# Optimization experiments

Hardware: AMD Instinct MI355X
Metric: run time of the kernel (lower is better)

The kernel has to match this reference:

```python
import jax, jax.numpy as jnp
import numpy as np

N, E, C, H, W = 5000, 80000, 32, 8, 8


def setup_inputs() -> dict:
    key = jax.random.key(0)
    k1, k2, k3, k4, k5, k6 = jax.random.split(key, 6)
    h = jax.random.normal(k1, (N, C, H, W), dtype=jnp.float32)
    e = jax.random.uniform(k2, (E,), dtype=jnp.float32)
    src = jax.random.randint(k3, (E,), 0, N, dtype=jnp.int32)
    # ensure every node receives at least one message (avoids -inf segments),
    # matching a connected graph where update_all covers all nodes
    dst = jnp.concatenate([jnp.arange(N, dtype=jnp.int32),
                           jax.random.randint(k4, (E - N,), 0, N, dtype=jnp.int32)])
    fan_in = C * 3 * 3
    bound = float(1.0 / np.sqrt(fan_in))
    conv_w = jax.random.uniform(k5, (C, C, 3, 3), minval=-bound, maxval=bound, dtype=jnp.float32)
    conv_b = jax.random.uniform(k6, (C,), minval=-bound, maxval=bound, dtype=jnp.float32)
    return {"h": h, "e": e, "conv_w": conv_w, "conv_b": conv_b, "src": src, "dst": dst}


def reference(h, e, conv_w, conv_b, src, dst):
    # message: gather source features per edge, scale by scalar edge weight
    m = e[:, None, None, None] * h[src]                      # [E, C, H, W]
    # conv2d(dim->dim, k=3, pad=1) + exact GELU, edges as batch dim
    m = jax.lax.conv_general_dilated(
        m, conv_w, window_strides=(1, 1), padding='SAME',
        dimension_numbers=('NCHW', 'OIHW', 'NCHW'))
    m = jax.nn.gelu(m + conv_b[None, :, None, None], approximate=False)
    # reduce: ragged max over each destination node's mailbox
    out = jax.ops.segment_max(m, dst, num_segments=h.shape[0])  # [N, C, H, W]
    return out
```

## Files before the change

kernel.cpp:

```cpp
#include <hip/hip_runtime.h>
#include <math.h>

#define CCH   32
#define HWPIX 64
#define CHW   2048
#define NHALF 2500
#define HT_STRIDE 40
#define HT_NODE   2600

typedef __attribute__((ext_vector_type(8))) short bf16x8;
typedef __attribute__((ext_vector_type(4))) float f32x4;
typedef unsigned int uint_t;
typedef unsigned short ushort_t;

__device__ __forceinline__ ushort_t f2bf(float f) {
    uint_t u = __float_as_uint(f);
    u += 0x7fffu + ((u >> 16) & 1u);
    return (ushort_t)(u >> 16);
}

__device__ __forceinline__ float fgelu(float x) {
    float x2 = x * x;
    float t = x * fmaf(0.0713548162726f, x2, 1.5957691216f);
    float ez = __expf(-t);
    return x * __builtin_amdgcn_rcpf(1.0f + ez);
}


__global__ __launch_bounds__(256) void hist_prep_kernel(
    const int* __restrict__ dst, int* cnt, int ne, int nhist,
    const float* __restrict__ w, ushort_t* __restrict__ wfrag) {
    int b = blockIdx.x;
    if (b < nhist) {
        int i = b * 256 + threadIdx.x;
        if (i < ne) atomicAdd(&cnt[dst[i]], 1);
    } else {
        for (int idx = threadIdx.x; idx < 18 * 64; idx += 256) {
            int ch = idx / (9 * 64);
            int rem = idx % (9 * 64);
            int tap = rem / 64;
            int l = rem % 64;
            int co = ch * 16 + (l & 15);
            int g = l >> 4;
            for (int j = 0; j < 8; j++) {
                int ci = g * 8 + j;
                wfrag[(size_t)idx * 8 + j] = f2bf(w[(co * CCH + ci) * 9 + tap]);
            }
        }
    }
}

__global__ __launch_bounds__(256) void scan_kernel(const int* __restrict__ cnt,
                                                   int* __restrict__ offs,
                                                   int* __restrict__ cursor,
                                                   int nn) {
    __shared__ int part[256];
    int t = threadIdx.x;
    int per = (nn + 255) >> 8;
    if (per > 32) per = 32;
    int base = t * per;
    int local[32];
    int sum = 0;
    for (int i = 0; i < per; i++) {
        int idx = base + i;
        int v = (idx < nn) ? cnt[idx] : 0;
        local[i] = sum;
        sum += v;
    }
    part[t] = sum;
    __syncthreads();
    int acc = sum;
    for (int d = 1; d < 256; d <<= 1) {
        int tv = (t >= d) ? part[t - d] : 0;
        __syncthreads();
        acc += tv;
        part[t] = acc;
        __syncthreads();
    }
    int excl = acc - sum;
    for (int i = 0; i < per; i++) {
        int idx = base + i;
        if (idx < nn) {
            int o = excl + local[i];
            offs[idx] = o;
            cursor[idx] = o;
        }
    }
    if (t == 255) offs[nn] = acc;
}

__global__ __launch_bounds__(256) void conv_scatter_kernel(
    const float* __restrict__ h, const ushort_t* __restrict__ wfrag,
    ushort_t* __restrict__ convh, int nconv,
    const int* __restrict__ dst, const int* __restrict__ src,
    const float* __restrict__ e, int* cursor, int2* __restrict__ swA, int ne) {
    __shared__ ushort_t Ht[2 * HT_NODE];
    int b = blockIdx.x;
    int t = threadIdx.x;

    if (b >= nconv) {
        int i = (b - nconv) * 256 + t;
        if (i < ne) {
            int p = atomicAdd(&cursor[dst[i]], 1);
            int2 v;
            v.x = src[i];
            v.y = __float_as_int(e[i]);
            swA[p] = v;
        }
        return;
    }

    int node0 = b * 2;
    uint_t* Hd = (uint_t*)Ht;
#pragma unroll
    for (int nd = 0; nd < 2; nd++) {
        const float* hn = h + (size_t)(node0 + nd) * CHW;
#pragma unroll
        for (int it = 0; it < 4; it++) {
            int ci2 = it * 4 + (t >> 6);
            int p = t & 63;
            float a = hn[ci2 * 128 + p];
            float bb = hn[ci2 * 128 + 64 + p];
            uint_t val = (uint_t)f2bf(a) | ((uint_t)f2bf(bb) << 16);
            Hd[nd * (HT_NODE / 2) + p * (HT_STRIDE / 2) + ci2] = val;
        }
    }
    if (t < 40) Hd[0 * (HT_NODE / 2) + 64 * (HT_STRIDE / 2) + (t % 20)] = 0;
    if (t >= 40 && t < 80) Hd[1 * (HT_NODE / 2) + 64 * (HT_STRIDE / 2) + (t - 40) % 20] = 0;
    __syncthreads();

    int l = t & 63;
    int w = __builtin_amdgcn_readfirstlane(t >> 6);
    int nd = w >> 1;
    int ch = w & 1;
    int s = l & 15, g = l >> 4;
    int n = node0 + nd;

    bf16x8 A[9];
#pragma unroll
    for (int tap = 0; tap < 9; tap++)
        A[tap] = ((const bf16x8*)wfrag)[(ch * 9 + tap) * 64 + l];

    f32x4 C[4];
#pragma unroll
    for (int i = 0; i < 4; i++) C[i] = (f32x4){0.f, 0.f, 0.f, 0.f};

    const short* HtS = (const short*)(Ht + nd * HT_NODE);
#pragma unroll
    for (int tau = 0; tau < 4; tau++) {
        int p = tau * 16 + s;
        int y = p >> 3, x = p & 7;
#pragma unroll
        for (int tap = 0; tap < 9; tap++) {
            int dy = tap / 3 - 1, dx = tap % 3 - 1;
            int yy = y + dy, xx = x + dx;
            bool valid = (yy >= 0) & (yy < 8) & (xx >= 0) & (xx < 8);
            int pp = valid ? (yy * 8 + xx) : 64;
            bf16x8 B = *(const bf16x8*)&HtS[pp * HT_STRIDE + g * 8];
            C[tau] = __builtin_amdgcn_mfma_f32_16x16x32_bf16(A[tap], B, C[tau], 0, 0, 0);
        }
    }

    ushort_t* outn = convh + (size_t)n * CHW;
#pragma unroll
    for (int tau = 0; tau < 4; tau++) {
        uint_t lo = (uint_t)f2bf(C[tau][0]) | ((uint_t)f2bf(C[tau][1]) << 16);
        uint_t hi = (uint_t)f2bf(C[tau][2]) | ((uint_t)f2bf(C[tau][3]) << 16);
        uint2 v; v.x = lo; v.y = hi;
        *(uint2*)(outn + (tau * 16 + s) * 32 + ch * 16 + g * 4) = v;
    }
}

__device__ __forceinline__ void red8(float* mn, float* mx, uint4 q, float wg) {
    uint_t u0 = q.x, u1 = q.y, u2 = q.z, u3 = q.w;
    float v;
    v = wg * __uint_as_float(u0 << 16);          mn[0] = fminf(mn[0], v); mx[0] = fmaxf(mx[0], v);
    v = wg * __uint_as_float(u0 & 0xffff0000u);  mn[1] = fminf(mn[1], v); mx[1] = fmaxf(mx[1], v);
    v = wg * __uint_as_float(u1 << 16);          mn[2] = fminf(mn[2], v); mx[2] = fmaxf(mx[2], v);
    v = wg * __uint_as_float(u1 & 0xffff0000u);  mn[3] = fminf(mn[3], v); mx[3] = fmaxf(mx[3], v);
    v = wg * __uint_as_float(u2 << 16);          mn[4] = fminf(mn[4], v); mx[4] = fmaxf(mx[4], v);
    v = wg * __uint_as_float(u2 & 0xffff0000u);  mn[5] = fminf(mn[5], v); mx[5] = fmaxf(mx[5], v);
    v = wg * __uint_as_float(u3 << 16);          mn[6] = fminf(mn[6], v); mx[6] = fmaxf(mx[6], v);
    v = wg * __uint_as_float(u3 & 0xffff0000u);  mn[7] = fminf(mn[7], v); mx[7] = fmaxf(mx[7], v);
}

__global__ __launch_bounds__(256) void gather_max_kernel(
    const ushort_t* __restrict__ convh, const float* __restrict__ bias,
    const int* __restrict__ offs, const int2* __restrict__ swA,
    float* __restrict__ out) {
    int t = threadIdx.x;
    int l = t & 63;
    int w = t >> 6;
    int b = blockIdx.x;
    int q = b & 3;
    int half = (b >> 2) & 1;
    int n = half * NHALF + (b >> 3) * 4 + w;
    int beg = offs[n], end = offs[n + 1];
    int last = end - 1;

    const char* qbase = (const char*)convh + 1024 * q + 16 * l;

    float mn[8], mx[8];
#pragma unroll
    for (int i = 0; i < 8; i++) { mn[i] = 3.402823466e+38f; mx[i] = -3.402823466e+38f; }

    int j1 = (beg + 1 < last) ? beg + 1 : last;
    int j2 = (beg + 2 < last) ? beg + 2 : last;
    int j3 = (beg + 3 < last) ? beg + 3 : last;
    int2 d0 = swA[beg], d1 = swA[j1], d2 = swA[j2], d3 = swA[j3];
    uint4 Q0 = *(const uint4*)(qbase + (size_t)d0.x * 4096);
    uint4 Q1 = *(const uint4*)(qbase + (size_t)d1.x * 4096);
    uint4 Q2 = *(const uint4*)(qbase + (size_t)d2.x * 4096);
    uint4 Q3 = *(const uint4*)(qbase + (size_t)d3.x * 4096);
    float W0 = __int_as_float(d0.y), W1 = __int_as_float(d1.y);
    float W2 = __int_as_float(d2.y), W3 = __int_as_float(d3.y);
    int k0 = (beg + 4 < last) ? beg + 4 : last;
    int k1 = (beg + 5 < last) ? beg + 5 : last;
    int k2 = (beg + 6 < last) ? beg + 6 : last;
    int k3 = (beg + 7 < last) ? beg + 7 : last;
    int2 S0 = swA[k0], S1 = swA[k1], S2 = swA[k2], S3 = swA[k3];

    for (int j = beg; j < end; j += 4) {
        int m0 = (j + 8 < last) ? j + 8 : last;
        int m1 = (j + 9 < last) ? j + 9 : last;
        int m2 = (j + 10 < last) ? j + 10 : last;
        int m3 = (j + 11 < last) ? j + 11 : last;
        int2 N0 = swA[m0], N1 = swA[m1], N2 = swA[m2], N3 = swA[m3];
        red8(mn, mx, Q0, W0);
        Q0 = *(const uint4*)(qbase + (size_t)S0.x * 4096); W0 = __int_as_float(S0.y);
        red8(mn, mx, Q1, W1);
        Q1 = *(const uint4*)(qbase + (size_t)S1.x * 4096); W1 = __int_as_float(S1.y);
        red8(mn, mx, Q2, W2);
        Q2 = *(const uint4*)(qbase + (size_t)S2.x * 4096); W2 = __int_as_float(S2.y);
        red8(mn, mx, Q3, W3);
        Q3 = *(const uint4*)(qbase + (size_t)S3.x * 4096); W3 = __int_as_float(S3.y);
        S0 = N0; S1 = N1; S2 = N2; S3 = N3;
    }

    const float4* b4 = (const float4*)(bias + (l & 3) * 8);
    float4 bLo = b4[0], bHi = b4[1];
    float bb[8] = {bLo.x, bLo.y, bLo.z, bLo.w, bHi.x, bHi.y, bHi.z, bHi.w};
    float* op = out + (size_t)n * CHW + (size_t)(l & 3) * 512 + q * 16 + (l >> 2);
#pragma unroll
    for (int i = 0; i < 8; i++) {
        op[i * 64] = fmaxf(fgelu(mx[i] + bb[i]), fgelu(mn[i] + bb[i]));
    }
}

extern "C" void kernel_launch(void* const* d_in, const int* in_sizes, int n_in,
                              void* d_out, int out_size, void* d_ws, size_t ws_size,
                              hipStream_t stream) {
    const float* h      = (const float*)d_in[0];
    const float* e      = (const float*)d_in[1];
    const float* conv_w = (const float*)d_in[2];
    const float* conv_b = (const float*)d_in[3];
    const int*   src    = (const int*)d_in[4];
    const int*   dst    = (const int*)d_in[5];
    int nn = in_sizes[0] / CHW;
    int ne = in_sizes[1];

    ushort_t* convh = (ushort_t*)d_ws;
    ushort_t* wfrag = convh + (size_t)nn * CHW;
    int*   cnt    = (int*)(wfrag + 18 * 64 * 8);
    int*   offs   = cnt + nn;
    int*   cursor = offs + nn + 2;
    int2*  swA    = (int2*)(cursor + nn);

    int nhist = (ne + 255) / 256;
    int nconv = nn / 2;

    hipMemsetAsync(cnt, 0, (size_t)nn * sizeof(int), stream);
    hist_prep_kernel<<<nhist + 1, 256, 0, stream>>>(dst, cnt, ne, nhist,
                                                    conv_w, wfrag);
    scan_kernel<<<1, 256, 0, stream>>>(cnt, offs, cursor, nn);
    conv_scatter_kernel<<<nconv + nhist, 256, 0, stream>>>(
        h, wfrag, convh, nconv, dst, src, e, cursor, swA, ne);
    gather_max_kernel<<<nn, 256, 0, stream>>>(convh, conv_b, offs, swA,
                                              (float*)d_out);
}
```

Before: 155.7 us.

## Store conv output as fp16 and reduce with packed half min/max

The conv kernel now writes its output as fp16 pairs (round-toward-zero pack) instead of bf16. The gather kernel then does the weight multiply and the min/max reduction with packed v_pk_mul/min/max f16 instructions, halving the ALU work per element. The gather prefetch is also deepened from 4 to 8 loads in flight, and the node index is made wave-uniform with readfirstlane. The risks are fp16 range and precision loss on conv outputs and weights, plus higher register pressure from the deeper prefetch.

Result: faster. 150.3 us (-3.5%).

```diff
diff --git a/kernel.cpp b/kernel.cpp
--- a/kernel.cpp
+++ b/kernel.cpp
@@ -10,6 +10,7 @@
 
 typedef __attribute__((ext_vector_type(8))) short bf16x8;
 typedef __attribute__((ext_vector_type(4))) float f32x4;
+typedef __fp16 fp16x2 __attribute__((ext_vector_type(2)));
 typedef unsigned int uint_t;
 typedef unsigned short ushort_t;
 
@@ -18,6 +19,21 @@
     u += 0x7fffu + ((u >> 16) & 1u);
     return (ushort_t)(u >> 16);
 }
+
+__device__ __forceinline__ uint_t pkh2(float a, float b) {
+    fp16x2 p = __builtin_amdgcn_cvt_pkrtz(a, b);
+    uint_t u;
+    __builtin_memcpy(&u, &p, 4);
+    return u;
+}
+
+__device__ __forceinline__ float h_lo(uint_t u) {
+    ushort_t s = (ushort_t)u;
+    __fp16 h;
+    __builtin_memcpy(&h, &s, 2);
+    return (float)h;
+}
+__device__ __forceinline__ float h_hi(uint_t u) { return h_lo(u >> 16); }
 
 __device__ __forceinline__ float fgelu(float x) {
     float x2 = x * x;
@@ -164,24 +180,24 @@
     ushort_t* outn = convh + (size_t)n * CHW;
 #pragma unroll
     for (int tau = 0; tau < 4; tau++) {
-        uint_t lo = (uint_t)f2bf(C[tau][0]) | ((uint_t)f2bf(C[tau][1]) << 16);
-        uint_t hi = (uint_t)f2bf(C[tau][2]) | ((uint_t)f2bf(C[tau][3]) << 16);
-        uint2 v; v.x = lo; v.y = hi;
+        uint2 v;
+        v.x = pkh2(C[tau][0], C[tau][1]);
+        v.y = pkh2(C[tau][2], C[tau][3]);
         *(uint2*)(outn + (tau * 16 + s) * 32 + ch * 16 + g * 4) = v;
     }
 }
 
-__device__ __forceinline__ void red8(float* mn, float* mx, uint4 q, float wg) {
-    uint_t u0 = q.x, u1 = q.y, u2 = q.z, u3 = q.w;
-    float v;
-    v = wg * __uint_as_float(u0 << 16);          mn[0] = fminf(mn[0], v); mx[0] = fmaxf(mx[0], v);
-    v = wg * __uint_as_float(u0 & 0xffff0000u);  mn[1] = fminf(mn[1], v); mx[1] = fmaxf(mx[1], v);
-    v = wg * __uint_as_float(u1 << 16);          mn[2] = fminf(mn[2], v); mx[2] = fmaxf(mx[2], v);
-    v = wg * __uint_as_float(u1 & 0xffff0000u);  mn[3] = fminf(mn[3], v); mx[3] = fmaxf(mx[3], v);
-    v = wg * __uint_as_float(u2 << 16);          mn[4] = fminf(mn[4], v); mx[4] = fmaxf(mx[4], v);
-    v = wg * __uint_as_float(u2 & 0xffff0000u);  mn[5] = fminf(mn[5], v); mx[5] = fmaxf(mx[5], v);
-    v = wg * __uint_as_float(u3 << 16);          mn[6] = fminf(mn[6], v); mx[6] = fmaxf(mx[6], v);
-    v = wg * __uint_as_float(u3 & 0xffff0000u);  mn[7] = fminf(mn[7], v); mx[7] = fmaxf(mx[7], v);
+__device__ __forceinline__ void red2h(uint_t* mn, uint_t* mx, uint_t d, uint_t w2) {
+    uint_t v;
+    asm("v_pk_mul_f16 %0, %1, %2" : "=v"(v) : "v"(d), "v"(w2));
+    asm("v_pk_min_f16 %0, %0, %1" : "+v"(*mn) : "v"(v));
+    asm("v_pk_max_f16 %0, %0, %1" : "+v"(*mx) : "v"(v));
+}
+__device__ __forceinline__ void red8h(uint_t* mn, uint_t* mx, uint4 qv, uint_t w2) {
+    red2h(&mn[0], &mx[0], qv.x, w2);
+    red2h(&mn[1], &mx[1], qv.y, w2);
+    red2h(&mn[2], &mx[2], qv.z, w2);
+    red2h(&mn[3], &mx[3], qv.w, w2);
 }
 
 __global__ __launch_bounds__(256) void gather_max_kernel(
@@ -194,47 +210,49 @@
     int b = blockIdx.x;
     int q = b & 3;
     int half = (b >> 2) & 1;
-    int n = half * NHALF + (b >> 3) * 4 + w;
+    int n = __builtin_amdgcn_readfirstlane(half * NHALF + (b >> 3) * 4 + w);
     int beg = offs[n], end = offs[n + 1];
     int last = end - 1;
 
     const char* qbase = (const char*)convh + 1024 * q + 16 * l;
 
-    float mn[8], mx[8];
-#pragma unroll
-    for (int i = 0; i < 8; i++) { mn[i] = 3.402823466e+38f; mx[i] = -3.402823466e+38f; }
-
-    int j1 = (beg + 1 < last) ? beg + 1 : last;
-    int j2 = (beg + 2 < last) ? beg + 2 : last;
-    int j3 = (beg + 3 < last) ? beg + 3 : last;
-    int2 d0 = swA[beg], d1 = swA[j1], d2 = swA[j2], d3 = swA[j3];
-    uint4 Q0 = *(const uint4*)(qbase + (size_t)d0.x * 4096);
-    uint4 Q1 = *(const uint4*)(qbase + (size_t)d1.x * 4096);
-    uint4 Q2 = *(const uint4*)(qbase + (size_t)d2.x * 4096);
-    uint4 Q3 = *(const uint4*)(qbase + (size_t)d3.x * 4096);
-    float W0 = __int_as_float(d0.y), W1 = __int_as_float(d1.y);
-    float W2 = __int_as_float(d2.y), W3 = __int_as_float(d3.y);
-    int k0 = (beg + 4 < last) ? beg + 4 : last;
-    int k1 = (beg + 5 < last) ? beg + 5 : last;
-    int k2 = (beg + 6 < last) ? beg + 6 : last;
-    int k3 = (beg + 7 < last) ? beg + 7 : last;
-    int2 S0 = swA[k0], S1 = swA[k1], S2 = swA[k2], S3 = swA[k3];
-
-    for (int j = beg; j < end; j += 4) {
-        int m0 = (j + 8 < last) ? j + 8 : last;
-        int m1 = (j + 9 < last) ? j + 9 : last;
-        int m2 = (j + 10 < last) ? j + 10 : last;
-        int m3 = (j + 11 < last) ? j + 11 : last;
-        int2 N0 = swA[m0], N1 = swA[m1], N2 = swA[m2], N3 = swA[m3];
-        red8(mn, mx, Q0, W0);
-        Q0 = *(const uint4*)(qbase + (size_t)S0.x * 4096); W0 = __int_as_float(S0.y);
-        red8(mn, mx, Q1, W1);
-        Q1 = *(const uint4*)(qbase + (size_t)S1.x * 4096); W1 = __int_as_float(S1.y);
-        red8(mn, mx, Q2, W2);
-        Q2 = *(const uint4*)(qbase + (size_t)S2.x * 4096); W2 = __int_as_float(S2.y);
-        red8(mn, mx, Q3, W3);
-        Q3 = *(const uint4*)(qbase + (size_t)S3.x * 4096); W3 = __int_as_float(S3.y);
-        S0 = N0; S1 = N1; S2 = N2; S3 = N3;
+    uint_t mn[4], mx[4];
+#pragma unroll
+    for (int i = 0; i < 4; i++) { mn[i] = 0x7c007c00u; mx[i] = 0xfc00fc00u; }
+
+    uint4 D[8];
+    uint_t Wh[8];
+    int2 T[8];
+#pragma unroll
+    for (int k = 0; k < 8; k++) {
+        int idx = beg + k; idx = idx < last ? idx : last;
+        int2 d = swA[idx];
+        D[k] = *(const uint4*)(qbase + (size_t)d.x * 4096);
+        float wf = __int_as_float(d.y);
+        Wh[k] = pkh2(wf, wf);
+    }
+#pragma unroll
+    for (int k = 0; k < 8; k++) {
+        int idx = beg + 8 + k; idx = idx < last ? idx : last;
+        T[k] = swA[idx];
+    }
+
+    for (int j = beg; j < end; j += 8) {
+        int2 U[8];
+#pragma unroll
+        for (int k = 0; k < 8; k++) {
+            int idx = j + 16 + k; idx = idx < last ? idx : last;
+            U[k] = swA[idx];
+        }
+#pragma unroll
+        for (int k = 0; k < 8; k++) {
+            red8h(mn, mx, D[k], Wh[k]);
+            D[k] = *(const uint4*)(qbase + (size_t)T[k].x * 4096);
+            float wf = __int_as_float(T[k].y);
+            Wh[k] = pkh2(wf, wf);
+        }
+#pragma unroll
+        for (int k = 0; k < 8; k++) T[k] = U[k];
     }
 
     const float4* b4 = (const float4*)(bias + (l & 3) * 8);
@@ -242,8 +260,11 @@
     float bb[8] = {bLo.x, bLo.y, bLo.z, bLo.w, bHi.x, bHi.y, bHi.z, bHi.w};
     float* op = out + (size_t)n * CHW + (size_t)(l & 3) * 512 + q * 16 + (l >> 2);
 #pragma unroll
-    for (int i = 0; i < 8; i++) {
-        op[i * 64] = fmaxf(fgelu(mx[i] + bb[i]), fgelu(mn[i] + bb[i]));
+    for (int k = 0; k < 4; k++) {
+        float mx0 = h_lo(mx[k]), mx1 = h_hi(mx[k]);
+        float mn0 = h_lo(mn[k]), mn1 = h_hi(mn[k]);
+        op[(2 * k) * 64]     = fmaxf(fgelu(mx0 + bb[2 * k]),     fgelu(mn0 + bb[2 * k]));
+        op[(2 * k + 1) * 64] = fmaxf(fgelu(mx1 + bb[2 * k + 1]), fgelu(mn1 + bb[2 * k + 1]));
     }
 }
 
@@ -269,7 +290,7 @@
     int nhist = (ne + 255) / 256;
     int nconv = nn / 2;
 
-    hipMemsetAsync(cnt, 0, (size_t)nn * sizeof(int), stream);
+    (void)hipMemsetAsync(cnt, 0, (size_t)nn * sizeof(int), stream);
     hist_prep_kernel<<<nhist + 1, 256, 0, stream>>>(dst, cnt, ne, nhist,
                                                     conv_w, wfrag);
     scan_kernel<<<1, 256, 0, stream>>>(cnt, offs, cursor, nn);
```
